# Kernel optimization log

Measured on AMD Instinct MI355X. Metric: run time of the kernel, lower is better.

## Reference

```python
import jax, jax.numpy as jnp
import numpy as np

SP_BETA = 1.0       # rendering_options.sp_beta
INF_DELTA = 1e10    # use_inf_depth=True -> last delta is 1e10
EPS = 1e-10


def setup_inputs() -> dict:
    key = jax.random.key(0)
    k1, k2, k3 = jax.random.split(key, 3)
    B, R, S, C = 8, 16384, 64, 3  # batch, rays, samples-per-ray, rgb channels
    colors = jax.random.normal(k1, (B, R, S, C), dtype=jnp.float32)
    densities = jax.random.normal(k2, (B, R, S, 1), dtype=jnp.float32)
    # depths must be sorted (increasing) along the sample dimension
    depths = jnp.sort(
        jax.random.uniform(k3, (B, R, S, 1), dtype=jnp.float32, minval=0.1, maxval=6.0),
        axis=2,
    )
    return {"colors": colors, "densities": densities, "depths": depths}


def reference(colors, densities, depths):
    # deltas between consecutive samples, last delta = 1e10 (infinite far plane)
    deltas = depths[:, :, 1:] - depths[:, :, :-1]                      # [B,R,S-1,1]
    deltas = jnp.concatenate(
        [deltas, jnp.full_like(deltas[:, :, :1], INF_DELTA)], axis=2)  # [B,R,S,1]

    # clamp_mode == 'softplus' with beta=1.0: softplus(x*beta)/beta
    dens = jax.nn.softplus(densities * SP_BETA) / SP_BETA              # [B,R,S,1]

    alphas = 1.0 - jnp.exp(-deltas * dens)                             # [B,R,S,1]

    # transmittance: cumulative product of (1-alpha), with leading ones
    trans = jnp.cumprod(1.0 - alphas + EPS, axis=2)                    # [B,R,S,1]
    trans = jnp.concatenate([jnp.ones_like(trans[:, :, :1]), trans], axis=2)  # [B,R,S+1,1]

    final_transmittance = trans[:, :, -1, 0]                           # [B,R]
    weights = alphas * trans[:, :, :-1]                                # [B,R,S,1]

    rgb_final = (weights * colors).sum(axis=2)                         # [B,R,C]
    depth = (weights * depths).sum(axis=2)                             # [B,R,1]
    return rgb_final, depth, weights, final_transmittance
```

## Files before the change

### kernel.cpp

```cpp
#include <hip/hip_runtime.h>

#define INF_DELTA 1e10f
#define LOG2E 1.4426950408889634f
#define LOG2_EPS -33.219280948873623f

typedef float floatx4 __attribute__((ext_vector_type(4)));

template<int CTRL, int RMASK>
__device__ __forceinline__ float dpp0(float v) {
    return __int_as_float(
        __builtin_amdgcn_update_dpp(0, __float_as_int(v), CTRL, RMASK, 0xF, false));
}

__device__ __forceinline__ float log2_softplus(float x) {
    const float q  = __builtin_amdgcn_exp2f(-__builtin_fabsf(x) * LOG2E);
    const float l2 = __builtin_amdgcn_logf(1.0f + q);
    return __builtin_fmaf(__builtin_fmaxf(x, 0.0f), LOG2E, l2);
}

__global__ __launch_bounds__(256) void raymarch_kernel(
    const float* __restrict__ colors,
    const float* __restrict__ densities,
    const float* __restrict__ depths,
    float* __restrict__ rgb_out,
    float* __restrict__ depth_out,
    float* __restrict__ weights_out,
    float* __restrict__ trans_out,
    int n_rays)
{
    const int lane = threadIdx.x & 63;
    const int wid  = threadIdx.x >> 6;
    const int nblk = n_rays >> 2;
    const int nw   = gridDim.x * 4;
    int t = blockIdx.x * 4 + wid;
    if (t >= nblk) return;

    long fb = (long)t * 256;
    float4 d4 = *reinterpret_cast<const float4*>(depths    + fb + lane * 4);
    float4 x4 = *reinterpret_cast<const float4*>(densities + fb + lane * 4);
    const float* cp0 = colors + fb * 3 + lane * 12;
    float4 ca = *reinterpret_cast<const float4*>(cp0);
    float4 cb = *reinterpret_cast<const float4*>(cp0 + 4);
    float4 cc = *reinterpret_cast<const float4*>(cp0 + 8);

    while (t < nblk) {
        const int  tn  = t + nw;
        const long fbn = (long)((tn < nblk) ? tn : t) * 256;
        const float4 d4n = *reinterpret_cast<const float4*>(depths    + fbn + lane * 4);
        const float4 x4n = *reinterpret_cast<const float4*>(densities + fbn + lane * 4);
        const float* cpn = colors + fbn * 3 + lane * 12;
        const float4 can = *reinterpret_cast<const float4*>(cpn);
        const float4 cbn = *reinterpret_cast<const float4*>(cpn + 4);
        const float4 ccn = *reinterpret_cast<const float4*>(cpn + 8);

        const long fbase = (long)t * 256;

        const float dnx  = dpp0<0x101, 0xF>(d4.x);
        const float del0 = d4.y - d4.x;
        const float del1 = d4.z - d4.y;
        const float del2 = d4.w - d4.z;
        const float del3 = ((lane & 15) == 15) ? INF_DELTA : (dnx - d4.w);

        const float g0 = -del0 * log2_softplus(x4.x);
        const float g1 = -del1 * log2_softplus(x4.y);
        const float g2 = -del2 * log2_softplus(x4.z);
        const float g3 = -del3 * log2_softplus(x4.w);
        const float a0 = 1.0f - __builtin_amdgcn_exp2f(g0);
        const float a1 = 1.0f - __builtin_amdgcn_exp2f(g1);
        const float a2 = 1.0f - __builtin_amdgcn_exp2f(g2);
        const float a3 = 1.0f - __builtin_amdgcn_exp2f(g3);
        const float l0 = __builtin_fmaxf(g0, LOG2_EPS);
        const float l1 = __builtin_fmaxf(g1, LOG2_EPS);
        const float l2 = __builtin_fmaxf(g2, LOG2_EPS);
        const float l3 = __builtin_fmaxf(g3, LOG2_EPS);

        const float L0 = l0;
        const float L1 = L0 + l1;
        const float L2 = L1 + l2;
        const float L3 = L2 + l3;
        float p = L3;
        p += dpp0<0x111, 0xF>(p);
        p += dpp0<0x112, 0xF>(p);
        p += dpp0<0x114, 0xF>(p);
        p += dpp0<0x118, 0xF>(p);
        const float excl = p - L3;

        const float e0 = __builtin_amdgcn_exp2f(excl);
        const float e1 = __builtin_amdgcn_exp2f(excl + L0);
        const float e2 = __builtin_amdgcn_exp2f(excl + L1);
        const float e3 = __builtin_amdgcn_exp2f(excl + L2);

        const float w0 = a0 * e0;
        const float w1 = a1 * e1;
        const float w2 = a2 * e2;
        const float w3 = a3 * e3;

        floatx4 wv; wv.x = w0; wv.y = w1; wv.z = w2; wv.w = w3;
        __builtin_nontemporal_store(wv,
            reinterpret_cast<floatx4*>(weights_out + fbase + lane * 4));

        float p0 = w0 * ca.x + w1 * ca.w + w2 * cb.z + w3 * cc.y;
        float p1 = w0 * ca.y + w1 * cb.x + w2 * cb.w + w3 * cc.z;
        float p2 = w0 * ca.z + w1 * cb.y + w2 * cc.x + w3 * cc.w;
        float p3 = w0 * d4.x + w1 * d4.y + w2 * d4.z + w3 * d4.w;

        p0 += dpp0<0xB1, 0xF>(p0);
        p1 += dpp0<0xB1, 0xF>(p1);
        p2 += dpp0<0xB1, 0xF>(p2);
        p3 += dpp0<0xB1, 0xF>(p3);
        p0 += dpp0<0x4E, 0xF>(p0);
        p1 += dpp0<0x4E, 0xF>(p1);
        p2 += dpp0<0x4E, 0xF>(p2);
        p3 += dpp0<0x4E, 0xF>(p3);

        const int c   = lane & 15;
        const int sel = lane & 3;
        float v = (sel == 0) ? p0 : (sel == 1) ? p1 : (sel == 2) ? p2 : p3;
        v += dpp0<0x124, 0xF>(v);
        v += dpp0<0x128, 0xF>(v);

        const int ray = t * 4 + (lane >> 4);
        if (c < 3) {
            __builtin_nontemporal_store(v, rgb_out + (long)ray * 3 + c);
        } else if (c == 3) {
            __builtin_nontemporal_store(v, depth_out + ray);
        }
        if (c == 15) {
            __builtin_nontemporal_store(__builtin_amdgcn_exp2f(p), trans_out + ray);
        }

        d4 = d4n; x4 = x4n; ca = can; cb = cbn; cc = ccn;
        t = tn;
    }
}

extern "C" void kernel_launch(void* const* d_in, const int* in_sizes, int n_in,
                              void* d_out, int out_size, void* d_ws, size_t ws_size,
                              hipStream_t stream) {
    const float* colors    = (const float*)d_in[0];
    const float* densities = (const float*)d_in[1];
    const float* depths    = (const float*)d_in[2];

    const int n_rays = in_sizes[1] / 64;

    float* out      = (float*)d_out;
    float* rgb      = out;
    float* depth_o  = rgb + (long)n_rays * 3;
    float* weights  = depth_o + n_rays;
    float* trans    = weights + (long)n_rays * 64;

    const int nblk = n_rays / 4;
    int blocks = 2048;
    if (blocks > (nblk + 3) / 4) blocks = (nblk + 3) / 4;
    raymarch_kernel<<<blocks, 256, 0, stream>>>(
        colors, densities, depths, rgb, depth_o, weights, trans, n_rays);
}
```

Measured before the change: 208.3 us.

## Coalesce color loads via LDS transpose with nontemporal loads and fewer blocks

```diff
diff --git a/kernel.cpp b/kernel.cpp
--- a/kernel.cpp
+++ b/kernel.cpp
@@ -18,6 +18,8 @@
     return __builtin_fmaf(__builtin_fmaxf(x, 0.0f), LOG2E, l2);
 }
 
+__device__ __forceinline__ int unit_off(int u) { return 4 * (u + (u >> 3)); }
+
 __global__ __launch_bounds__(256) void raymarch_kernel(
     const float* __restrict__ colors,
     const float* __restrict__ densities,
@@ -28,6 +30,8 @@
     float* __restrict__ trans_out,
     int n_rays)
 {
+    __shared__ float lds[4][216 * 4];
+
     const int lane = threadIdx.x & 63;
     const int wid  = threadIdx.x >> 6;
     const int nblk = n_rays >> 2;
@@ -35,25 +39,49 @@
     int t = blockIdx.x * 4 + wid;
     if (t >= nblk) return;
 
+    float* wbuf = lds[wid];
+
     long fb = (long)t * 256;
-    float4 d4 = *reinterpret_cast<const float4*>(depths    + fb + lane * 4);
-    float4 x4 = *reinterpret_cast<const float4*>(densities + fb + lane * 4);
-    const float* cp0 = colors + fb * 3 + lane * 12;
-    float4 ca = *reinterpret_cast<const float4*>(cp0);
-    float4 cb = *reinterpret_cast<const float4*>(cp0 + 4);
-    float4 cc = *reinterpret_cast<const float4*>(cp0 + 8);
+    const float* cb0 = colors + fb * 3;
+    floatx4 ch0 = __builtin_nontemporal_load(
+        reinterpret_cast<const floatx4*>(cb0 + (0 * 64 + lane) * 4));
+    floatx4 ch1 = __builtin_nontemporal_load(
+        reinterpret_cast<const floatx4*>(cb0 + (1 * 64 + lane) * 4));
+    floatx4 ch2 = __builtin_nontemporal_load(
+        reinterpret_cast<const floatx4*>(cb0 + (2 * 64 + lane) * 4));
+    floatx4 d4 = __builtin_nontemporal_load(
+        reinterpret_cast<const floatx4*>(depths    + fb + lane * 4));
+    floatx4 x4 = __builtin_nontemporal_load(
+        reinterpret_cast<const floatx4*>(densities + fb + lane * 4));
 
-    while (t < nblk) {
-        const int  tn  = t + nw;
-        const long fbn = (long)((tn < nblk) ? tn : t) * 256;
-        const float4 d4n = *reinterpret_cast<const float4*>(depths    + fbn + lane * 4);
-        const float4 x4n = *reinterpret_cast<const float4*>(densities + fbn + lane * 4);
-        const float* cpn = colors + fbn * 3 + lane * 12;
-        const float4 can = *reinterpret_cast<const float4*>(cpn);
-        const float4 cbn = *reinterpret_cast<const float4*>(cpn + 4);
-        const float4 ccn = *reinterpret_cast<const float4*>(cpn + 8);
+    while (true) {
+        const int  tn   = t + nw;
+        const bool more = (tn < nblk);
+
+        floatx4 nch0, nch1, nch2, nd4, nx4;
+        if (more) {
+            const long fbn = (long)tn * 256;
+            const float* cbn = colors + fbn * 3;
+            nch0 = __builtin_nontemporal_load(
+                reinterpret_cast<const floatx4*>(cbn + (0 * 64 + lane) * 4));
+            nch1 = __builtin_nontemporal_load(
+                reinterpret_cast<const floatx4*>(cbn + (1 * 64 + lane) * 4));
+            nch2 = __builtin_nontemporal_load(
+                reinterpret_cast<const floatx4*>(cbn + (2 * 64 + lane) * 4));
+            nd4 = __builtin_nontemporal_load(
+                reinterpret_cast<const floatx4*>(depths    + fbn + lane * 4));
+            nx4 = __builtin_nontemporal_load(
+                reinterpret_cast<const floatx4*>(densities + fbn + lane * 4));
+        }
 
         const long fbase = (long)t * 256;
+
+        *reinterpret_cast<floatx4*>(wbuf + unit_off(0 * 64 + lane)) = ch0;
+        *reinterpret_cast<floatx4*>(wbuf + unit_off(1 * 64 + lane)) = ch1;
+        *reinterpret_cast<floatx4*>(wbuf + unit_off(2 * 64 + lane)) = ch2;
+        const floatx4 ca = *reinterpret_cast<const floatx4*>(wbuf + unit_off(3 * lane));
+        const floatx4 cbv = *reinterpret_cast<const floatx4*>(wbuf + unit_off(3 * lane + 1));
+        const floatx4 cc = *reinterpret_cast<const floatx4*>(wbuf + unit_off(3 * lane + 2));
 
         const float dnx  = dpp0<0x101, 0xF>(d4.x);
         const float del0 = d4.y - d4.x;
@@ -99,10 +127,10 @@
         __builtin_nontemporal_store(wv,
             reinterpret_cast<floatx4*>(weights_out + fbase + lane * 4));
 
-        float p0 = w0 * ca.x + w1 * ca.w + w2 * cb.z + w3 * cc.y;
-        float p1 = w0 * ca.y + w1 * cb.x + w2 * cb.w + w3 * cc.z;
-        float p2 = w0 * ca.z + w1 * cb.y + w2 * cc.x + w3 * cc.w;
-        float p3 = w0 * d4.x + w1 * d4.y + w2 * d4.z + w3 * d4.w;
+        float p0 = w0 * ca.x  + w1 * ca.w  + w2 * cbv.z + w3 * cc.y;
+        float p1 = w0 * ca.y  + w1 * cbv.x + w2 * cbv.w + w3 * cc.z;
+        float p2 = w0 * ca.z  + w1 * cbv.y + w2 * cc.x  + w3 * cc.w;
+        float p3 = w0 * d4.x  + w1 * d4.y  + w2 * d4.z  + w3 * d4.w;
 
         p0 += dpp0<0xB1, 0xF>(p0);
         p1 += dpp0<0xB1, 0xF>(p1);
@@ -129,7 +157,8 @@
             __builtin_nontemporal_store(__builtin_amdgcn_exp2f(p), trans_out + ray);
         }
 
-        d4 = d4n; x4 = x4n; ca = can; cb = cbn; cc = ccn;
+        if (!more) break;
+        ch0 = nch0; ch1 = nch1; ch2 = nch2; d4 = nd4; x4 = nx4;
         t = tn;
     }
 }
@@ -150,7 +179,7 @@
     float* trans    = weights + (long)n_rays * 64;
 
     const int nblk = n_rays / 4;
-    int blocks = 2048;
+    int blocks = 1024;
     if (blocks > (nblk + 3) / 4) blocks = (nblk + 3) / 4;
     raymarch_kernel<<<blocks, 256, 0, stream>>>(
         colors, densities, depths, rgb, depth_o, weights, trans, n_rays);
```

Result: faster. 192.3 us (-7.7%).
